# Performance work log

Hardware: AMD Instinct MI355X
Metric: run time of the kernel (lower is better)

The kernel has to match this reference:

```python
import jax, jax.numpy as jnp
import numpy as np

N = 2560          # 64 graphs * 40 nodes (hard-coded by view(64,40,40))
E = 163840        # edges, avg degree 64
HEADS = 4
IN_C = 32
H0 = 128          # hidden_dims[0] per head
H1 = 128          # hidden_dims[1] per head
OUT_E = 40
EPS_BN = 1e-5


def _glorot(key, shape):
    fan = sum(shape[-2:]) if len(shape) > 1 else shape[0]
    return jax.random.normal(key, shape, dtype=jnp.float32) * (2.0 / fan) ** 0.5


def setup_inputs() -> dict:
    key = jax.random.key(0)
    ks = jax.random.split(key, 24)
    inp = {
        "x": jax.random.normal(ks[0], (N, IN_C), dtype=jnp.float32),
        "edge_index": jax.random.randint(ks[1], (2, E), 0, N, dtype=jnp.int32),
        "pos": jax.random.normal(ks[2], (N, 2), dtype=jnp.float32),
        "mask": jax.random.randint(ks[3], (N,), 0, 2, dtype=jnp.int32),
        "adjacency": jax.random.uniform(ks[4], (N, OUT_E), dtype=jnp.float32),
        # GAT layer 1 (in -> heads*H0)
        "W1": _glorot(ks[5], (IN_C, HEADS * H0)),
        "att_src1": _glorot(ks[6], (HEADS, H0)),
        "att_dst1": _glorot(ks[7], (HEADS, H0)),
        "We1": _glorot(ks[8], (1, HEADS * H0)),
        "att_e1": _glorot(ks[9], (HEADS, H0)),
        "bias1": jnp.zeros((HEADS * H0,), dtype=jnp.float32),
        # BatchNorm 1
        "g1": jnp.ones((HEADS * H0,), dtype=jnp.float32),
        "be1": jnp.zeros((HEADS * H0,), dtype=jnp.float32),
        # GAT layer 2 (heads*H0 -> heads*H1)
        "W2": _glorot(ks[10], (HEADS * H0, HEADS * H1)),
        "att_src2": _glorot(ks[11], (HEADS, H1)),
        "att_dst2": _glorot(ks[12], (HEADS, H1)),
        "We2": _glorot(ks[13], (1, HEADS * H1)),
        "att_e2": _glorot(ks[14], (HEADS, H1)),
        "bias2": jnp.zeros((HEADS * H1,), dtype=jnp.float32),
        # BatchNorm 2
        "g2": jnp.ones((HEADS * H1,), dtype=jnp.float32),
        "be2": jnp.zeros((HEADS * H1,), dtype=jnp.float32),
        # fc_edge
        "Wfc": _glorot(ks[15], (HEADS * H1, OUT_E)),
        "bfc": jnp.zeros((OUT_E,), dtype=jnp.float32),
    }
    return inp


def _gat(x, src, dst, ew, W, att_s, att_d, We, att_e, bias, heads, c):
    # x: [N, Fin] -> h: [N, H, C]
    h = (x @ W).reshape(-1, heads, c)
    a_s = (h * att_s).sum(-1)                       # [N, H]
    a_d = (h * att_d).sum(-1)                       # [N, H]
    he = (ew[:, None] @ We).reshape(-1, heads, c)   # [E, H, C] edge attr proj
    a_e = (he * att_e).sum(-1)                      # [E, H]
    alpha = jax.nn.leaky_relu(a_s[src] + a_d[dst] + a_e, 0.2)
    # segment softmax over destination nodes
    m = jax.ops.segment_max(alpha, dst, num_segments=N)
    alpha = jnp.exp(alpha - m[dst])
    denom = jax.ops.segment_sum(alpha, dst, num_segments=N)
    alpha = alpha / (denom[dst] + 1e-16)
    out = jax.ops.segment_sum(h[src] * alpha[:, :, None], dst, num_segments=N)
    return out.reshape(-1, heads * c) + bias


def _batchnorm(x, g, b):
    mu = x.mean(0)
    var = x.var(0)
    return (x - mu) * jax.lax.rsqrt(var + EPS_BN) * g + b


def reference(x, edge_index, pos, mask, adjacency,
              W1, att_src1, att_dst1, We1, att_e1, bias1, g1, be1,
              W2, att_src2, att_dst2, We2, att_e2, bias2, g2, be2,
              Wfc, bfc):
    src, dst = edge_index[0], edge_index[1]
    ew = 1.0 / (jnp.linalg.norm(pos[src] - pos[dst], axis=1) + 1e-6)  # [E]

    h = _gat(x, src, dst, ew, W1, att_src1, att_dst1, We1, att_e1, bias1, HEADS, H0)
    h = jax.nn.relu(_batchnorm(h, g1, be1))

    e = _gat(h, src, dst, ew, W2, att_src2, att_dst2, We2, att_e2, bias2, HEADS, H1)
    e = jax.nn.relu(_batchnorm(e, g2, be2))

    out_edge = e @ Wfc + bfc                     # [N, 40]
    out_edge = out_edge * mask[:, None].astype(out_edge.dtype)
    out_edge = out_edge.reshape(64, 40, 40)
    return out_edge + adjacency.reshape(64, 40, 40)
```

## Files before the change

kernel.cpp:

```cpp
#include <hip/hip_runtime.h>
#include <hip/hip_bf16.h>

#define NN 2560
#define NE 163840
#define NH 4
#define NC 128
#define NF 512
#define OUTE 40
#define CSTR 256

typedef short bf16x8 __attribute__((ext_vector_type(8)));
typedef float f32x4 __attribute__((ext_vector_type(4)));

__device__ inline ushort f2bf(float f) {
    uint u = __float_as_uint(f);
    uint r = u + 0x7FFF + ((u >> 16) & 1);
    return (ushort)(r >> 16);
}
__device__ inline float bflo(uint v) { return __uint_as_float(v << 16); }
__device__ inline float bfhi(uint v) { return __uint_as_float(v & 0xFFFF0000u); }
__device__ inline float bf2f(ushort u) { return __uint_as_float(((uint)u) << 16); }
__device__ inline float rdlanef(float v, int l) {
    return __int_as_float(__builtin_amdgcn_readlane(__float_as_int(v), l));
}
__device__ inline int rdlanei(int v, int l) {
    return __builtin_amdgcn_readlane(v, l);
}
__device__ inline float sel4(float r0, float r1, float r2, float r3, int hd) {
    return (hd & 2) ? ((hd & 1) ? r3 : r2) : ((hd & 1) ? r1 : r0);
}

__global__ __launch_bounds__(256) void k_csr_gemm1(const int* __restrict__ ei,
        const float* __restrict__ pos, int* __restrict__ deg,
        int2* __restrict__ csrp, int* __restrict__ ovf_cnt, int4* __restrict__ ovf,
        const float* __restrict__ We1, const float* __restrict__ ae1,
        const float* __restrict__ We2, const float* __restrict__ ae2,
        float* __restrict__ dote,
        const float* __restrict__ Wfc, ushort* __restrict__ WfcT,
        const float* __restrict__ W2, ushort* __restrict__ W2T,
        const float* __restrict__ x, const float* __restrict__ W1,
        const float* __restrict__ atts, const float* __restrict__ attd,
        ushort* __restrict__ hb, float* __restrict__ as_, float* __restrict__ ad_) {
    __shared__ ushort tile[64][72];
    __shared__ float s_x[4][32];
    __shared__ float4 s_red[4][4];
    int b = blockIdx.x;
    if (b < 640) {
        int e = b * 256 + threadIdx.x;
        int s = ei[e], d = ei[NE + e];
        float dx = pos[2 * s] - pos[2 * d];
        float dy = pos[2 * s + 1] - pos[2 * d + 1];
        float w = 1.0f / (sqrtf(dx * dx + dy * dy) + 1e-6f);
        int r = atomicAdd(&deg[d], 1);
        if (r < CSTR) {
            csrp[(d << 8) + r] = make_int2(s, __float_as_int(w));
        } else {
            int i = atomicAdd(ovf_cnt, 1);
            ovf[i] = make_int4(d, s, __float_as_int(w), 0);
        }
        return;
    }
    if (b < 642) {
        int t = threadIdx.x;
        const float* W = (b == 641) ? We2 : We1;
        const float* A = (b == 641) ? ae2 : ae1;
        int w = t >> 6, l = t & 63;
        float p = W[w * 128 + l] * A[w * 128 + l] + W[w * 128 + 64 + l] * A[w * 128 + 64 + l];
#pragma unroll
        for (int o = 32; o > 0; o >>= 1) p += __shfl_down(p, o);
        if (l == 0) dote[(b - 640) * 4 + w] = p;
        return;
    }
    if (b < 738) {
        int idx = (b - 642) * 256 + threadIdx.x;
        int j = idx >> 9, k = idx & 511;
        WfcT[idx] = (j < OUTE) ? f2bf(Wfc[k * OUTE + j]) : (ushort)0;
        return;
    }
    if (b < 802) {
        int id = b - 738;
        int n0 = (id & 7) * 64, k0 = (id >> 3) * 64;
        int t = threadIdx.x;
        int r = t >> 2, cseg = (t & 3) * 16;
#pragma unroll
        for (int c = 0; c < 16; c += 4) {
            float4 v = *(const float4*)&W2[(k0 + r) * 512 + n0 + cseg + c];
            tile[cseg + c + 0][r] = f2bf(v.x);
            tile[cseg + c + 1][r] = f2bf(v.y);
            tile[cseg + c + 2][r] = f2bf(v.z);
            tile[cseg + c + 3][r] = f2bf(v.w);
        }
        __syncthreads();
        *(uint4*)&W2T[(n0 + r) * 512 + k0 + cseg]     = *(uint4*)&tile[r][cseg];
        *(uint4*)&W2T[(n0 + r) * 512 + k0 + cseg + 8] = *(uint4*)&tile[r][cseg + 8];
        return;
    }
    int n0 = (b - 802) * 4, t = threadIdx.x;
    if (t < 128) s_x[t >> 5][t & 31] = x[n0 * 32 + t];
    __syncthreads();
    float a0[4] = {0.f, 0.f, 0.f, 0.f}, a1[4] = {0.f, 0.f, 0.f, 0.f};
#pragma unroll
    for (int k = 0; k < 32; k++) {
        float w0 = W1[k * 512 + t];
        float w1 = W1[k * 512 + t + 256];
#pragma unroll
        for (int nn = 0; nn < 4; nn++) {
            a0[nn] += s_x[nn][k] * w0;
            a1[nn] += s_x[nn][k] * w1;
        }
    }
    float sa0 = atts[t], sa1 = atts[t + 256];
    float da0 = attd[t], da1 = attd[t + 256];
    int w = t >> 6, lane = t & 63;
#pragma unroll
    for (int nn = 0; nn < 4; nn++) {
        hb[(n0 + nn) * 512 + t] = f2bf(a0[nn]);
        hb[(n0 + nn) * 512 + t + 256] = f2bf(a1[nn]);
        float ps0 = a0[nn] * sa0, pd0 = a0[nn] * da0;
        float ps1 = a1[nn] * sa1, pd1 = a1[nn] * da1;
#pragma unroll
        for (int o = 32; o > 0; o >>= 1) {
            ps0 += __shfl_xor(ps0, o); pd0 += __shfl_xor(pd0, o);
            ps1 += __shfl_xor(ps1, o); pd1 += __shfl_xor(pd1, o);
        }
        if (lane == 0) s_red[w][nn] = make_float4(ps0, pd0, ps1, pd1);
    }
    __syncthreads();
    if (t < 4) {
        int nn = t, n = n0 + nn;
        float4 r0 = s_red[0][nn], r1 = s_red[1][nn], r2 = s_red[2][nn], r3 = s_red[3][nn];
        as_[n * 4 + 0] = r0.x + r1.x; as_[n * 4 + 1] = r2.x + r3.x;
        as_[n * 4 + 2] = r0.z + r1.z; as_[n * 4 + 3] = r2.z + r3.z;
        ad_[n * 4 + 0] = r0.y + r1.y; ad_[n * 4 + 1] = r2.y + r3.y;
        ad_[n * 4 + 2] = r0.w + r1.w; ad_[n * 4 + 3] = r2.w + r3.w;
    }
}

__global__ __launch_bounds__(128) void k_edge_agg(const int* __restrict__ deg_,
        const int2* __restrict__ csrp, const int* __restrict__ ovf_cnt,
        const int4* __restrict__ ovf, const float* __restrict__ as_,
        const float* __restrict__ ad_, const float* __restrict__ dote,
        const ushort* __restrict__ hb, const float* __restrict__ bias,
        ushort* __restrict__ outb) {
    int w = threadIdx.x >> 6, lane = threadIdx.x & 63;
    int n = blockIdx.x * 2 + w;
    int beg = n << 8;
    int degn = deg_[n];
    int dmain = min(degn, CSTR);
    float4 adv = *(const float4*)&ad_[n * 4];
    float4 dv  = *(const float4*)dote;
    float La0 = -1e30f, La1 = -1e30f, La2 = -1e30f, La3 = -1e30f;
    float Lb0 = -1e30f, Lb1 = -1e30f, Lb2 = -1e30f, Lb3 = -1e30f;
    int off0 = 0, off1 = 0;
    if (lane < dmain) {
        int2 p = csrp[beg + lane];
        off0 = p.x * NF;
        float4 a = *(const float4*)&as_[p.x * 4];
        float ww = __int_as_float(p.y);
        float v0 = a.x + adv.x + ww * dv.x; La0 = v0 > 0.f ? v0 : 0.2f * v0;
        float v1 = a.y + adv.y + ww * dv.y; La1 = v1 > 0.f ? v1 : 0.2f * v1;
        float v2 = a.z + adv.z + ww * dv.z; La2 = v2 > 0.f ? v2 : 0.2f * v2;
        float v3 = a.w + adv.w + ww * dv.w; La3 = v3 > 0.f ? v3 : 0.2f * v3;
    }
    if (lane + 64 < dmain) {
        int2 p = csrp[beg + lane + 64];
        off1 = p.x * NF;
        float4 a = *(const float4*)&as_[p.x * 4];
        float ww = __int_as_float(p.y);
        float v0 = a.x + adv.x + ww * dv.x; Lb0 = v0 > 0.f ? v0 : 0.2f * v0;
        float v1 = a.y + adv.y + ww * dv.y; Lb1 = v1 > 0.f ? v1 : 0.2f * v1;
        float v2 = a.z + adv.z + ww * dv.z; Lb2 = v2 > 0.f ? v2 : 0.2f * v2;
        float v3 = a.w + adv.w + ww * dv.w; Lb3 = v3 > 0.f ? v3 : 0.2f * v3;
    }
    float mx0 = fmaxf(La0, Lb0), mx1 = fmaxf(La1, Lb1);
    float mx2 = fmaxf(La2, Lb2), mx3 = fmaxf(La3, Lb3);
    for (int e = 128 + lane; e < dmain; e += 64) {
        int2 p = csrp[beg + e];
        float4 a = *(const float4*)&as_[p.x * 4];
        float ww = __int_as_float(p.y);
        float v0 = a.x + adv.x + ww * dv.x; v0 = v0 > 0.f ? v0 : 0.2f * v0;
        float v1 = a.y + adv.y + ww * dv.y; v1 = v1 > 0.f ? v1 : 0.2f * v1;
        float v2 = a.z + adv.z + ww * dv.z; v2 = v2 > 0.f ? v2 : 0.2f * v2;
        float v3 = a.w + adv.w + ww * dv.w; v3 = v3 > 0.f ? v3 : 0.2f * v3;
        mx0 = fmaxf(mx0, v0); mx1 = fmaxf(mx1, v1);
        mx2 = fmaxf(mx2, v2); mx3 = fmaxf(mx3, v3);
    }
    if (degn > CSTR) {
        int oc = *ovf_cnt;
        for (int i = lane; i < oc; i += 64) {
            int4 o = ovf[i];
            if (o.x == n) {
                float4 a = *(const float4*)&as_[o.y * 4];
                float ww = __int_as_float(o.z);
                float v0 = a.x + adv.x + ww * dv.x; v0 = v0 > 0.f ? v0 : 0.2f * v0;
                float v1 = a.y + adv.y + ww * dv.y; v1 = v1 > 0.f ? v1 : 0.2f * v1;
                float v2 = a.z + adv.z + ww * dv.z; v2 = v2 > 0.f ? v2 : 0.2f * v2;
                float v3 = a.w + adv.w + ww * dv.w; v3 = v3 > 0.f ? v3 : 0.2f * v3;
                mx0 = fmaxf(mx0, v0); mx1 = fmaxf(mx1, v1);
                mx2 = fmaxf(mx2, v2); mx3 = fmaxf(mx3, v3);
            }
        }
    }
#pragma unroll
    for (int o = 32; o > 0; o >>= 1) {
        mx0 = fmaxf(mx0, __shfl_xor(mx0, o));
        mx1 = fmaxf(mx1, __shfl_xor(mx1, o));
        mx2 = fmaxf(mx2, __shfl_xor(mx2, o));
        mx3 = fmaxf(mx3, __shfl_xor(mx3, o));
    }
    float Aa0 = __expf(La0 - mx0), Aa1 = __expf(La1 - mx1);
    float Aa2 = __expf(La2 - mx2), Aa3 = __expf(La3 - mx3);
    float Ab0 = __expf(Lb0 - mx0), Ab1 = __expf(Lb1 - mx1);
    float Ab2 = __expf(Lb2 - mx2), Ab3 = __expf(Lb3 - mx3);
    float s0 = Aa0 + Ab0, s1 = Aa1 + Ab1, s2 = Aa2 + Ab2, s3 = Aa3 + Ab3;
    for (int e = 128 + lane; e < dmain; e += 64) {
        int2 p = csrp[beg + e];
        float4 a = *(const float4*)&as_[p.x * 4];
        float ww = __int_as_float(p.y);
        float v0 = a.x + adv.x + ww * dv.x; v0 = v0 > 0.f ? v0 : 0.2f * v0;
        float v1 = a.y + adv.y + ww * dv.y; v1 = v1 > 0.f ? v1 : 0.2f * v1;
        float v2 = a.z + adv.z + ww * dv.z; v2 = v2 > 0.f ? v2 : 0.2f * v2;
        float v3 = a.w + adv.w + ww * dv.w; v3 = v3 > 0.f ? v3 : 0.2f * v3;
        s0 += __expf(v0 - mx0); s1 += __expf(v1 - mx1);
        s2 += __expf(v2 - mx2); s3 += __expf(v3 - mx3);
    }
    if (degn > CSTR) {
        int oc = *ovf_cnt;
        for (int i = lane; i < oc; i += 64) {
            int4 o = ovf[i];
            if (o.x == n) {
                float4 a = *(const float4*)&as_[o.y * 4];
                float ww = __int_as_float(o.z);
                float v0 = a.x + adv.x + ww * dv.x; v0 = v0 > 0.f ? v0 : 0.2f * v0;
                float v1 = a.y + adv.y + ww * dv.y; v1 = v1 > 0.f ? v1 : 0.2f * v1;
                float v2 = a.z + adv.z + ww * dv.z; v2 = v2 > 0.f ? v2 : 0.2f * v2;
                float v3 = a.w + adv.w + ww * dv.w; v3 = v3 > 0.f ? v3 : 0.2f * v3;
                s0 += __expf(v0 - mx0); s1 += __expf(v1 - mx1);
                s2 += __expf(v2 - mx2); s3 += __expf(v3 - mx3);
            }
        }
    }
#pragma unroll
    for (int o = 32; o > 0; o >>= 1) {
        s0 += __shfl_xor(s0, o); s1 += __shfl_xor(s1, o);
        s2 += __shfl_xor(s2, o); s3 += __shfl_xor(s3, o);
    }
    float inv0 = 1.f / (s0 + 1e-16f), inv1 = 1.f / (s1 + 1e-16f);
    float inv2 = 1.f / (s2 + 1e-16f), inv3 = 1.f / (s3 + 1e-16f);
    int hd = lane >> 4;
    const ushort* hbase = hb + 8 * lane;
    float acc0 = 0.f, acc1 = 0.f, acc2 = 0.f, acc3 = 0.f;
    float acc4 = 0.f, acc5 = 0.f, acc6 = 0.f, acc7 = 0.f;
    int m0 = min(dmain, 64);
    int e = 0;
    for (; e + 8 <= m0; e += 8) {
        int o[8]; float aa[8];
#pragma unroll
        for (int j = 0; j < 8; j++) {
            o[j] = rdlanei(off0, e + j);
            float r0 = rdlanef(Aa0, e + j), r1 = rdlanef(Aa1, e + j);
            float r2 = rdlanef(Aa2, e + j), r3 = rdlanef(Aa3, e + j);
            aa[j] = sel4(r0, r1, r2, r3, hd);
        }
        uint4 v[8];
#pragma unroll
        for (int j = 0; j < 8; j++) v[j] = *(const uint4*)(hbase + o[j]);
#pragma unroll
        for (int j = 0; j < 8; j++) {
            acc0 += aa[j] * bflo(v[j].x); acc1 += aa[j] * bfhi(v[j].x);
            acc2 += aa[j] * bflo(v[j].y); acc3 += aa[j] * bfhi(v[j].y);
            acc4 += aa[j] * bflo(v[j].z); acc5 += aa[j] * bfhi(v[j].z);
            acc6 += aa[j] * bflo(v[j].w); acc7 += aa[j] * bfhi(v[j].w);
        }
    }
    for (; e < m0; e++) {
        float r0 = rdlanef(Aa0, e), r1 = rdlanef(Aa1, e);
        float r2 = rdlanef(Aa2, e), r3 = rdlanef(Aa3, e);
        float a = sel4(r0, r1, r2, r3, hd);
        int o = rdlanei(off0, e);
        uint4 v = *(const uint4*)(hbase + o);
        acc0 += a * bflo(v.x); acc1 += a * bfhi(v.x);
        acc2 += a * bflo(v.y); acc3 += a * bfhi(v.y);
        acc4 += a * bflo(v.z); acc5 += a * bfhi(v.z);
        acc6 += a * bflo(v.w); acc7 += a * bfhi(v.w);
    }
    int m1b = max(min(dmain, 128) - 64, 0);
    e = 0;
    for (; e + 8 <= m1b; e += 8) {
        int o[8]; float aa[8];
#pragma unroll
        for (int j = 0; j < 8; j++) {
            o[j] = rdlanei(off1, e + j);
            float r0 = rdlanef(Ab0, e + j), r1 = rdlanef(Ab1, e + j);
            float r2 = rdlanef(Ab2, e + j), r3 = rdlanef(Ab3, e + j);
            aa[j] = sel4(r0, r1, r2, r3, hd);
        }
        uint4 v[8];
#pragma unroll
        for (int j = 0; j < 8; j++) v[j] = *(const uint4*)(hbase + o[j]);
#pragma unroll
        for (int j = 0; j < 8; j++) {
            acc0 += aa[j] * bflo(v[j].x); acc1 += aa[j] * bfhi(v[j].x);
            acc2 += aa[j] * bflo(v[j].y); acc3 += aa[j] * bfhi(v[j].y);
            acc4 += aa[j] * bflo(v[j].z); acc5 += aa[j] * bfhi(v[j].z);
            acc6 += aa[j] * bflo(v[j].w); acc7 += aa[j] * bfhi(v[j].w);
        }
    }
    for (; e < m1b; e++) {
        float r0 = rdlanef(Ab0, e), r1 = rdlanef(Ab1, e);
        float r2 = rdlanef(Ab2, e), r3 = rdlanef(Ab3, e);
        float a = sel4(r0, r1, r2, r3, hd);
        int o = rdlanei(off1, e);
        uint4 v = *(const uint4*)(hbase + o);
        acc0 += a * bflo(v.x); acc1 += a * bfhi(v.x);
        acc2 += a * bflo(v.y); acc3 += a * bfhi(v.y);
        acc4 += a * bflo(v.z); acc5 += a * bfhi(v.z);
        acc6 += a * bflo(v.w); acc7 += a * bfhi(v.w);
    }
    float adh = sel4(adv.x, adv.y, adv.z, adv.w, hd);
    float dh  = sel4(dv.x, dv.y, dv.z, dv.w, hd);
    float mxh = sel4(mx0, mx1, mx2, mx3, hd);
    for (int ee = 128; ee < dmain; ee++) {
        int2 p = csrp[beg + ee];
        float ash = as_[p.x * 4 + hd];
        float ww = __int_as_float(p.y);
        float vv = ash + adh + ww * dh; vv = vv > 0.f ? vv : 0.2f * vv;
        float a = __expf(vv - mxh);
        uint4 v = *(const uint4*)(hbase + p.x * NF);
        acc0 += a * bflo(v.x); acc1 += a * bfhi(v.x);
        acc2 += a * bflo(v.y); acc3 += a * bfhi(v.y);
        acc4 += a * bflo(v.z); acc5 += a * bfhi(v.z);
        acc6 += a * bflo(v.w); acc7 += a * bfhi(v.w);
    }
    if (degn > CSTR) {
        int oc = *ovf_cnt;
        for (int i = 0; i < oc; i++) {
            int4 o = ovf[i];
            if (o.x == n) {
                float ash = as_[o.y * 4 + hd];
                float ww = __int_as_float(o.z);
                float vv = ash + adh + ww * dh; vv = vv > 0.f ? vv : 0.2f * vv;
                float a = __expf(vv - mxh);
                uint4 v = *(const uint4*)(hbase + o.y * NF);
                acc0 += a * bflo(v.x); acc1 += a * bfhi(v.x);
                acc2 += a * bflo(v.y); acc3 += a * bfhi(v.y);
                acc4 += a * bflo(v.z); acc5 += a * bfhi(v.z);
                acc6 += a * bflo(v.w); acc7 += a * bfhi(v.w);
            }
        }
    }
    float invh = sel4(inv0, inv1, inv2, inv3, hd);
    int ch = 8 * lane;
    float4 b0 = *(const float4*)&bias[ch];
    float4 b1 = *(const float4*)&bias[ch + 4];
    uint4 ov;
    ov.x = (uint)f2bf(acc0 * invh + b0.x) | ((uint)f2bf(acc1 * invh + b0.y) << 16);
    ov.y = (uint)f2bf(acc2 * invh + b0.z) | ((uint)f2bf(acc3 * invh + b0.w) << 16);
    ov.z = (uint)f2bf(acc4 * invh + b1.x) | ((uint)f2bf(acc5 * invh + b1.y) << 16);
    ov.w = (uint)f2bf(acc6 * invh + b1.z) | ((uint)f2bf(acc7 * invh + b1.w) << 16);
    *(uint4*)&outb[n * NF + ch] = ov;
}

__global__ __launch_bounds__(256) void k_bnstats(const ushort* __restrict__ xs,
        float* __restrict__ stats) {
    __shared__ float ps[2048];
    __shared__ float pq[2048];
    int t = threadIdx.x;
    int c8 = (t & 63) * 8, rr = t >> 6;
    float s[8] = {0.f,0.f,0.f,0.f,0.f,0.f,0.f,0.f};
    float q[8] = {0.f,0.f,0.f,0.f,0.f,0.f,0.f,0.f};
#pragma unroll
    for (int rj = 0; rj < 4; rj++) {
        int r = blockIdx.x * 16 + rr * 4 + rj;
        uint4 v = *(const uint4*)&xs[r * NF + c8];
        float vv[8];
        vv[0] = bflo(v.x); vv[1] = bfhi(v.x); vv[2] = bflo(v.y); vv[3] = bfhi(v.y);
        vv[4] = bflo(v.z); vv[5] = bfhi(v.z); vv[6] = bflo(v.w); vv[7] = bfhi(v.w);
#pragma unroll
        for (int c = 0; c < 8; c++) { s[c] += vv[c]; q[c] += vv[c] * vv[c]; }
    }
#pragma unroll
    for (int c = 0; c < 8; c++) {
        ps[rr * 512 + c8 + c] = s[c];
        pq[rr * 512 + c8 + c] = q[c];
    }
    __syncthreads();
    for (int ch = t; ch < 512; ch += 256) {
        atomicAdd(&stats[ch], ps[ch] + ps[512 + ch] + ps[1024 + ch] + ps[1536 + ch]);
        atomicAdd(&stats[NF + ch], pq[ch] + pq[512 + ch] + pq[1024 + ch] + pq[1536 + ch]);
    }
}

__global__ __launch_bounds__(256) void k_gemm2_bn_att(const ushort* __restrict__ Ab,
        const float* __restrict__ stats, const float* __restrict__ g,
        const float* __restrict__ bb, const ushort* __restrict__ BT,
        const float* __restrict__ atts, const float* __restrict__ attd,
        ushort* __restrict__ Cb, float* __restrict__ as_, float* __restrict__ ad_) {
    __shared__ ushort As[64][40];
    __shared__ ushort Bs[128][40];
    __shared__ float s_scale[512], s_shift[512];
    __shared__ float s_ps[2][64], s_pd[2][64];
    int t = threadIdx.x;
    const float invn = 1.0f / (float)NN;
    {
        int j = t;
#pragma unroll
        for (int rep = 0; rep < 2; rep++, j += 256) {
            float mu = stats[j] * invn;
            float var = stats[NF + j] * invn - mu * mu;
            float sc = rsqrtf(var + 1e-5f) * g[j];
            s_scale[j] = sc;
            s_shift[j] = bb[j] - mu * sc;
        }
    }
    int head = blockIdx.x;
    int rowBase = blockIdx.y * 64, colBase = head * 128;
    int w = t >> 6, lane = t & 63;
    int wm = (w >> 1) * 32, wn = (w & 1) * 64;
    int lm = lane & 15, q = lane >> 4;
    f32x4 acc[2][4] = {};
    int sr2 = t >> 2, sk = (t & 3) * 8;
    for (int k0 = 0; k0 < 512; k0 += 32) {
        __syncthreads();
        int jb = k0 + sk;
        float sc[8], sh[8];
#pragma unroll
        for (int c = 0; c < 8; c++) { sc[c] = s_scale[jb + c]; sh[c] = s_shift[jb + c]; }
        uint4 a8 = *(const uint4*)&Ab[(rowBase + sr2) * 512 + jb];
        uint4 b0 = *(const uint4*)&BT[(colBase + sr2) * 512 + jb];
        uint4 b1 = *(const uint4*)&BT[(colBase + 64 + sr2) * 512 + jb];
        ushort pa0[8];
        float av[8];
        av[0] = bflo(a8.x); av[1] = bfhi(a8.x); av[2] = bflo(a8.y); av[3] = bfhi(a8.y);
        av[4] = bflo(a8.z); av[5] = bfhi(a8.z); av[6] = bflo(a8.w); av[7] = bfhi(a8.w);
#pragma unroll
        for (int c = 0; c < 8; c++)
            pa0[c] = f2bf(fmaxf(av[c] * sc[c] + sh[c], 0.f));
        *(uint4*)&As[sr2][sk]      = *(uint4*)pa0;
        *(uint4*)&Bs[sr2][sk]      = b0;
        *(uint4*)&Bs[64 + sr2][sk] = b1;
        __syncthreads();
        bf16x8 af[2], bf[4];
#pragma unroll
        for (int i = 0; i < 2; i++) af[i] = *(const bf16x8*)&As[wm + i * 16 + lm][q * 8];
#pragma unroll
        for (int j = 0; j < 4; j++) bf[j] = *(const bf16x8*)&Bs[wn + j * 16 + lm][q * 8];
#pragma unroll
        for (int i = 0; i < 2; i++)
#pragma unroll
            for (int j = 0; j < 4; j++)
                acc[i][j] = __builtin_amdgcn_mfma_f32_16x16x32_bf16(af[i], bf[j], acc[i][j], 0, 0, 0);
    }
#pragma unroll
    for (int i = 0; i < 2; i++) {
        int row = rowBase + wm + i * 16 + q * 4;
#pragma unroll
        for (int j = 0; j < 4; j++) {
            int col = colBase + wn + j * 16 + lm;
#pragma unroll
            for (int r = 0; r < 4; r++)
                Cb[(row + r) * 512 + col] = f2bf(acc[i][j][r]);
        }
    }
    float sa[4], da[4];
#pragma unroll
    for (int j = 0; j < 4; j++) {
        int col = colBase + wn + j * 16 + lm;
        sa[j] = atts[col]; da[j] = attd[col];
    }
#pragma unroll
    for (int i = 0; i < 2; i++) {
#pragma unroll
        for (int r = 0; r < 4; r++) {
            float ps = 0.f, pd = 0.f;
#pragma unroll
            for (int j = 0; j < 4; j++) {
                float c = acc[i][j][r];
                ps += c * sa[j]; pd += c * da[j];
            }
#pragma unroll
            for (int o = 1; o < 16; o <<= 1) { ps += __shfl_xor(ps, o); pd += __shfl_xor(pd, o); }
            if (lm == 0) {
                int row = wm + i * 16 + q * 4 + r;
                s_ps[w & 1][row] = ps; s_pd[w & 1][row] = pd;
            }
        }
    }
    __syncthreads();
    if (t < 64) {
        as_[(rowBase + t) * 4 + head] = s_ps[0][t] + s_ps[1][t];
    } else if (t < 128) {
        int row = t - 64;
        ad_[(rowBase + row) * 4 + head] = s_pd[0][row] + s_pd[1][row];
    }
}

__global__ __launch_bounds__(256) void k_fc_bn(const ushort* __restrict__ e2b,
        const float* __restrict__ stats, const float* __restrict__ g,
        const float* __restrict__ bb, const ushort* __restrict__ WfcT,
        const float* __restrict__ bfc, const int* __restrict__ mask,
        const float* __restrict__ adj, float* __restrict__ out) {
    __shared__ float s_scale[512], s_shift[512];
    __shared__ f32x4 s_acc[3][64][3];
    int t = threadIdx.x;
    int w = t >> 6, lane = t & 63;
    const float invn = 1.0f / (float)NN;
#pragma unroll
    for (int j = t; j < 512; j += 256) {
        float mu = stats[j] * invn;
        float var = stats[NF + j] * invn - mu * mu;
        float sc = rsqrtf(var + 1e-5f) * g[j];
        s_scale[j] = sc;
        s_shift[j] = bb[j] - mu * sc;
    }
    __syncthreads();
    int r0 = blockIdx.x * 16;
    int lm = lane & 15, q = lane >> 4;
    f32x4 acc[3] = {};
#pragma unroll
    for (int kk = 0; kk < 4; kk++) {
        int k0 = w * 128 + kk * 32;
        int jb = k0 + q * 8;
        uint4 a8 = *(const uint4*)&e2b[(r0 + lm) * 512 + jb];
        float av[8];
        av[0] = bflo(a8.x); av[1] = bfhi(a8.x); av[2] = bflo(a8.y); av[3] = bfhi(a8.y);
        av[4] = bflo(a8.z); av[5] = bfhi(a8.z); av[6] = bflo(a8.w); av[7] = bfhi(a8.w);
        ushort pa[8];
#pragma unroll
        for (int c = 0; c < 8; c++)
            pa[c] = f2bf(fmaxf(av[c] * s_scale[jb + c] + s_shift[jb + c], 0.f));
        bf16x8 af = *(const bf16x8*)pa;
#pragma unroll
        for (int jt = 0; jt < 3; jt++) {
            bf16x8 bf = *(const bf16x8*)&WfcT[(jt * 16 + lm) * 512 + k0 + q * 8];
            acc[jt] = __builtin_amdgcn_mfma_f32_16x16x32_bf16(af, bf, acc[jt], 0, 0, 0);
        }
    }
    if (w > 0) {
#pragma unroll
        for (int jt = 0; jt < 3; jt++) s_acc[w - 1][lane][jt] = acc[jt];
    }
    __syncthreads();
    if (w == 0) {
#pragma unroll
        for (int jt = 0; jt < 3; jt++) {
            acc[jt] += s_acc[0][lane][jt] + s_acc[1][lane][jt] + s_acc[2][lane][jt];
            int col = jt * 16 + lm;
            if (col < OUTE) {
#pragma unroll
                for (int r = 0; r < 4; r++) {
                    int n = r0 + q * 4 + r;
                    float v = acc[jt][r] + bfc[col];
                    v = mask[n] ? v : 0.f;
                    out[n * OUTE + col] = v + adj[n * OUTE + col];
                }
            }
        }
    }
}

extern "C" void kernel_launch(void* const* d_in, const int* in_sizes, int n_in,
                              void* d_out, int out_size, void* d_ws, size_t ws_size,
                              hipStream_t stream) {
    const float* x       = (const float*)d_in[0];
    const int*   ei      = (const int*)d_in[1];
    const float* pos     = (const float*)d_in[2];
    const int*   mask    = (const int*)d_in[3];
    const float* adj     = (const float*)d_in[4];
    const float* W1      = (const float*)d_in[5];
    const float* atts1   = (const float*)d_in[6];
    const float* attd1   = (const float*)d_in[7];
    const float* We1     = (const float*)d_in[8];
    const float* atte1   = (const float*)d_in[9];
    const float* bias1   = (const float*)d_in[10];
    const float* g1      = (const float*)d_in[11];
    const float* be1     = (const float*)d_in[12];
    const float* W2      = (const float*)d_in[13];
    const float* atts2   = (const float*)d_in[14];
    const float* attd2   = (const float*)d_in[15];
    const float* We2     = (const float*)d_in[16];
    const float* atte2   = (const float*)d_in[17];
    const float* bias2   = (const float*)d_in[18];
    const float* g2      = (const float*)d_in[19];
    const float* be2     = (const float*)d_in[20];
    const float* Wfc     = (const float*)d_in[21];
    const float* bfc     = (const float*)d_in[22];
    float* out = (float*)d_out;

    char* ws = (char*)d_ws;
    int*    deg     = (int*)(ws);
    int*    ovf_cnt = (int*)(ws + 2560 * 4);
    float*  stats   = (float*)(ws + 5120 * 4);
    float*  dote    = (float*)(ws + 7168 * 4);
    int2*   csrp    = (int2*)(ws + 7184 * 4);
    int4*   ovf     = (int4*)(ws + 1317904 * 4);
    float*  as_     = (float*)(ws + 1973264 * 4);
    float*  ad_     = (float*)(ws + 1983504 * 4);
    ushort* t1b     = (ushort*)(ws + 1993744 * 4);
    ushort* hb      = (ushort*)(ws + 2649104 * 4);
    ushort* W2T     = (ushort*)(ws + 3304464 * 4);
    ushort* WfcT    = (ushort*)(ws + 3435536 * 4);

    hipMemsetAsync(d_ws, 0, 7168 * 4, stream);

    k_csr_gemm1<<<802 + NN / 4, 256, 0, stream>>>(ei, pos, deg, csrp, ovf_cnt, ovf,
                                                  We1, atte1, We2, atte2, dote,
                                                  Wfc, WfcT, W2, W2T,
                                                  x, W1, atts1, attd1, hb, as_, ad_);

    k_edge_agg<<<NN / 2, 128, 0, stream>>>(deg, csrp, ovf_cnt, ovf, as_, ad_,
                                           dote, hb, bias1, t1b);
    k_bnstats<<<NN / 16, 256, 0, stream>>>(t1b, stats);

    k_gemm2_bn_att<<<dim3(4, NN / 64), 256, 0, stream>>>(t1b, stats, g1, be1, W2T,
                                                         atts2, attd2, hb, as_, ad_);
    k_edge_agg<<<NN / 2, 128, 0, stream>>>(deg, csrp, ovf_cnt, ovf, as_, ad_,
                                           dote + 4, hb, bias2, t1b);
    k_bnstats<<<NN / 16, 256, 0, stream>>>(t1b, stats + 1024);

    k_fc_bn<<<NN / 16, 256, 0, stream>>>(t1b, stats + 1024, g2, be2, WfcT, bfc, mask, adj, out);
}
```

Baseline: 196.0 us.

## Fuse BN stats into consumer kernels via atomic counter spin-wait; stage alpha in LDS

The BatchNorm statistics kernels are merged into the following GEMM2 and FC kernels. The first 160 blocks compute the stats and bump an agent-scope done counter. The remaining blocks spin-wait on that counter, then read the stats with atomic loads, which removes two kernel launches. In edge aggregation, the CSR loads are hoisted and made unconditional with clamped indices, attention weights are staged in shared memory instead of being fetched with readlane and select per edge, and the first gather loop is unrolled to 16. The spin-wait relies on the stats blocks being scheduled before or alongside the waiting blocks, which risks deadlock or stalls if they are not.

Measured after the change: 209.3 us. 1.07x slower.

```diff
diff --git a/kernel.cpp b/kernel.cpp
--- a/kernel.cpp
+++ b/kernel.cpp
@@ -142,36 +142,41 @@
         const float* __restrict__ ad_, const float* __restrict__ dote,
         const ushort* __restrict__ hb, const float* __restrict__ bias,
         ushort* __restrict__ outb) {
+    __shared__ float s_alpha[2][2][4][72];
     int w = threadIdx.x >> 6, lane = threadIdx.x & 63;
     int n = blockIdx.x * 2 + w;
     int beg = n << 8;
+    int2 p0 = csrp[beg + lane];
+    int2 p1 = csrp[beg + 64 + lane];
     int degn = deg_[n];
-    int dmain = min(degn, CSTR);
     float4 adv = *(const float4*)&ad_[n * 4];
     float4 dv  = *(const float4*)dote;
-    float La0 = -1e30f, La1 = -1e30f, La2 = -1e30f, La3 = -1e30f;
-    float Lb0 = -1e30f, Lb1 = -1e30f, Lb2 = -1e30f, Lb3 = -1e30f;
-    int off0 = 0, off1 = 0;
-    if (lane < dmain) {
-        int2 p = csrp[beg + lane];
-        off0 = p.x * NF;
-        float4 a = *(const float4*)&as_[p.x * 4];
-        float ww = __int_as_float(p.y);
-        float v0 = a.x + adv.x + ww * dv.x; La0 = v0 > 0.f ? v0 : 0.2f * v0;
-        float v1 = a.y + adv.y + ww * dv.y; La1 = v1 > 0.f ? v1 : 0.2f * v1;
-        float v2 = a.z + adv.z + ww * dv.z; La2 = v2 > 0.f ? v2 : 0.2f * v2;
-        float v3 = a.w + adv.w + ww * dv.w; La3 = v3 > 0.f ? v3 : 0.2f * v3;
-    }
-    if (lane + 64 < dmain) {
-        int2 p = csrp[beg + lane + 64];
-        off1 = p.x * NF;
-        float4 a = *(const float4*)&as_[p.x * 4];
-        float ww = __int_as_float(p.y);
-        float v0 = a.x + adv.x + ww * dv.x; Lb0 = v0 > 0.f ? v0 : 0.2f * v0;
-        float v1 = a.y + adv.y + ww * dv.y; Lb1 = v1 > 0.f ? v1 : 0.2f * v1;
-        float v2 = a.z + adv.z + ww * dv.z; Lb2 = v2 > 0.f ? v2 : 0.2f * v2;
-        float v3 = a.w + adv.w + ww * dv.w; Lb3 = v3 > 0.f ? v3 : 0.2f * v3;
-    }
+    int i0 = min(max(p0.x, 0), NN - 1);
+    int i1 = min(max(p1.x, 0), NN - 1);
+    float4 a0 = *(const float4*)&as_[i0 * 4];
+    float4 a1 = *(const float4*)&as_[i1 * 4];
+    int dmain = min(degn, CSTR);
+    bool val0 = lane < dmain, val1 = lane + 64 < dmain;
+    float ww0 = __int_as_float(p0.y), ww1 = __int_as_float(p1.y);
+    float La0, La1, La2, La3, Lb0, Lb1, Lb2, Lb3;
+    {
+        float v0 = a0.x + adv.x + ww0 * dv.x; v0 = v0 > 0.f ? v0 : 0.2f * v0;
+        float v1 = a0.y + adv.y + ww0 * dv.y; v1 = v1 > 0.f ? v1 : 0.2f * v1;
+        float v2 = a0.z + adv.z + ww0 * dv.z; v2 = v2 > 0.f ? v2 : 0.2f * v2;
+        float v3 = a0.w + adv.w + ww0 * dv.w; v3 = v3 > 0.f ? v3 : 0.2f * v3;
+        La0 = val0 ? v0 : -1e30f; La1 = val0 ? v1 : -1e30f;
+        La2 = val0 ? v2 : -1e30f; La3 = val0 ? v3 : -1e30f;
+    }
+    {
+        float v0 = a1.x + adv.x + ww1 * dv.x; v0 = v0 > 0.f ? v0 : 0.2f * v0;
+        float v1 = a1.y + adv.y + ww1 * dv.y; v1 = v1 > 0.f ? v1 : 0.2f * v1;
+        float v2 = a1.z + adv.z + ww1 * dv.z; v2 = v2 > 0.f ? v2 : 0.2f * v2;
+        float v3 = a1.w + adv.w + ww1 * dv.w; v3 = v3 > 0.f ? v3 : 0.2f * v3;
+        Lb0 = val1 ? v0 : -1e30f; Lb1 = val1 ? v1 : -1e30f;
+        Lb2 = val1 ? v2 : -1e30f; Lb3 = val1 ? v3 : -1e30f;
+    }
+    int off0 = val0 ? i0 * NF : 0;
+    int off1 = val1 ? i1 * NF : 0;
     float mx0 = fmaxf(La0, Lb0), mx1 = fmaxf(La1, Lb1);
     float mx2 = fmaxf(La2, Lb2), mx3 = fmaxf(La3, Lb3);
     for (int e = 128 + lane; e < dmain; e += 64) {
@@ -247,36 +252,34 @@
     }
     float inv0 = 1.f / (s0 + 1e-16f), inv1 = 1.f / (s1 + 1e-16f);
     float inv2 = 1.f / (s2 + 1e-16f), inv3 = 1.f / (s3 + 1e-16f);
+    s_alpha[w][0][0][lane] = Aa0; s_alpha[w][0][1][lane] = Aa1;
+    s_alpha[w][0][2][lane] = Aa2; s_alpha[w][0][3][lane] = Aa3;
+    s_alpha[w][1][0][lane] = Ab0; s_alpha[w][1][1][lane] = Ab1;
+    s_alpha[w][1][2][lane] = Ab2; s_alpha[w][1][3][lane] = Ab3;
     int hd = lane >> 4;
     const ushort* hbase = hb + 8 * lane;
     float acc0 = 0.f, acc1 = 0.f, acc2 = 0.f, acc3 = 0.f;
     float acc4 = 0.f, acc5 = 0.f, acc6 = 0.f, acc7 = 0.f;
     int m0 = min(dmain, 64);
     int e = 0;
-    for (; e + 8 <= m0; e += 8) {
-        int o[8]; float aa[8];
-#pragma unroll
-        for (int j = 0; j < 8; j++) {
-            o[j] = rdlanei(off0, e + j);
-            float r0 = rdlanef(Aa0, e + j), r1 = rdlanef(Aa1, e + j);
-            float r2 = rdlanef(Aa2, e + j), r3 = rdlanef(Aa3, e + j);
-            aa[j] = sel4(r0, r1, r2, r3, hd);
-        }
-        uint4 v[8];
-#pragma unroll
-        for (int j = 0; j < 8; j++) v[j] = *(const uint4*)(hbase + o[j]);
-#pragma unroll
-        for (int j = 0; j < 8; j++) {
-            acc0 += aa[j] * bflo(v[j].x); acc1 += aa[j] * bfhi(v[j].x);
-            acc2 += aa[j] * bflo(v[j].y); acc3 += aa[j] * bfhi(v[j].y);
-            acc4 += aa[j] * bflo(v[j].z); acc5 += aa[j] * bfhi(v[j].z);
-            acc6 += aa[j] * bflo(v[j].w); acc7 += aa[j] * bfhi(v[j].w);
+    for (; e + 16 <= m0; e += 16) {
+        int o[16];
+#pragma unroll
+        for (int j = 0; j < 16; j++) o[j] = rdlanei(off0, e + j);
+        uint4 v[16];
+#pragma unroll
+        for (int j = 0; j < 16; j++) v[j] = *(const uint4*)(hbase + o[j]);
+#pragma unroll
+        for (int j = 0; j < 16; j++) {
+            float a = s_alpha[w][0][hd][e + j];
+            acc0 += a * bflo(v[j].x); acc1 += a * bfhi(v[j].x);
+            acc2 += a * bflo(v[j].y); acc3 += a * bfhi(v[j].y);
+            acc4 += a * bflo(v[j].z); acc5 += a * bfhi(v[j].z);
+            acc6 += a * bflo(v[j].w); acc7 += a * bfhi(v[j].w);
         }
     }
     for (; e < m0; e++) {
-        float r0 = rdlanef(Aa0, e), r1 = rdlanef(Aa1, e);
-        float r2 = rdlanef(Aa2, e), r3 = rdlanef(Aa3, e);
-        float a = sel4(r0, r1, r2, r3, hd);
+        float a = s_alpha[w][0][hd][e];
         int o = rdlanei(off0, e);
         uint4 v = *(const uint4*)(hbase + o);
         acc0 += a * bflo(v.x); acc1 += a * bfhi(v.x);
@@ -287,29 +290,23 @@
     int m1b = max(min(dmain, 128) - 64, 0);
     e = 0;
     for (; e + 8 <= m1b; e += 8) {
-        int o[8]; float aa[8];
+        int o[8];
+#pragma unroll
+        for (int j = 0; j < 8; j++) o[j] = rdlanei(off1, e + j);
+        uint4 v[8];
+#pragma unroll
+        for (int j = 0; j < 8; j++) v[j] = *(const uint4*)(hbase + o[j]);
 #pragma unroll
         for (int j = 0; j < 8; j++) {
-            o[j] = rdlanei(off1, e + j);
-            float r0 = rdlanef(Ab0, e + j), r1 = rdlanef(Ab1, e + j);
-            float r2 = rdlanef(Ab2, e + j), r3 = rdlanef(Ab3, e + j);
-            aa[j] = sel4(r0, r1, r2, r3, hd);
-        }
-        uint4 v[8];
-#pragma unroll
-        for (int j = 0; j < 8; j++) v[j] = *(const uint4*)(hbase + o[j]);
-#pragma unroll
-        for (int j = 0; j < 8; j++) {
-            acc0 += aa[j] * bflo(v[j].x); acc1 += aa[j] * bfhi(v[j].x);
-            acc2 += aa[j] * bflo(v[j].y); acc3 += aa[j] * bfhi(v[j].y);
-            acc4 += aa[j] * bflo(v[j].z); acc5 += aa[j] * bfhi(v[j].z);
-            acc6 += aa[j] * bflo(v[j].w); acc7 += aa[j] * bfhi(v[j].w);
+            float a = s_alpha[w][1][hd][e + j];
+            acc0 += a * bflo(v[j].x); acc1 += a * bfhi(v[j].x);
+            acc2 += a * bflo(v[j].y); acc3 += a * bfhi(v[j].y);
+            acc4 += a * bflo(v[j].z); acc5 += a * bfhi(v[j].z);
+            acc6 += a * bflo(v[j].w); acc7 += a * bfhi(v[j].w);
         }
     }
     for (; e < m1b; e++) {
-        float r0 = rdlanef(Ab0, e), r1 = rdlanef(Ab1, e);
-        float r2 = rdlanef(Ab2, e), r3 = rdlanef(Ab3, e);
-        float a = sel4(r0, r1, r2, r3, hd);
+        float a = s_alpha[w][1][hd][e];
         int o = rdlanei(off1, e);
         uint4 v = *(const uint4*)(hbase + o);
         acc0 += a * bflo(v.x); acc1 += a * bfhi(v.x);
@@ -361,10 +358,10 @@
     *(uint4*)&outb[n * NF + ch] = ov;
 }
 
-__global__ __launch_bounds__(256) void k_bnstats(const ushort* __restrict__ xs,
-        float* __restrict__ stats) {
-    __shared__ float ps[2048];
-    __shared__ float pq[2048];
+__device__ __forceinline__ void bnstats_body(char* smem, const ushort* __restrict__ xs,
+        float* __restrict__ stats, int* done) {
+    float* ps = (float*)smem;
+    float* pq = (float*)(smem + 8192);
     int t = threadIdx.x;
     int c8 = (t & 63) * 8, rr = t >> 6;
     float s[8] = {0.f,0.f,0.f,0.f,0.f,0.f,0.f,0.f};
@@ -389,32 +386,52 @@
         atomicAdd(&stats[ch], ps[ch] + ps[512 + ch] + ps[1024 + ch] + ps[1536 + ch]);
         atomicAdd(&stats[NF + ch], pq[ch] + pq[512 + ch] + pq[1024 + ch] + pq[1536 + ch]);
     }
-}
-
-__global__ __launch_bounds__(256) void k_gemm2_bn_att(const ushort* __restrict__ Ab,
-        const float* __restrict__ stats, const float* __restrict__ g,
+    __syncthreads();
+    if (t == 0)
+        __hip_atomic_fetch_add(done, 1, __ATOMIC_RELEASE, __HIP_MEMORY_SCOPE_AGENT);
+}
+
+__device__ __forceinline__ void wait_done(const int* done, int target) {
+    if (threadIdx.x == 0) {
+        while (__hip_atomic_load((int*)done, __ATOMIC_ACQUIRE, __HIP_MEMORY_SCOPE_AGENT) < target)
+            __builtin_amdgcn_s_sleep(8);
+    }
+    __syncthreads();
+}
+__device__ __forceinline__ float ld_agent(const float* p) {
+    return __hip_atomic_load((float*)p, __ATOMIC_RELAXED, __HIP_MEMORY_SCOPE_AGENT);
+}
+
+__global__ __launch_bounds__(256) void k_stats_gemm2(const ushort* __restrict__ Ab,
+        float* __restrict__ stats, int* done, const float* __restrict__ g,
         const float* __restrict__ bb, const ushort* __restrict__ BT,
         const float* __restrict__ atts, const float* __restrict__ attd,
         ushort* __restrict__ Cb, float* __restrict__ as_, float* __restrict__ ad_) {
-    __shared__ ushort As[64][40];
-    __shared__ ushort Bs[128][40];
-    __shared__ float s_scale[512], s_shift[512];
-    __shared__ float s_ps[2][64], s_pd[2][64];
+    __shared__ __align__(16) char smem[20480];
+    if (blockIdx.x < 160) { bnstats_body(smem, Ab, stats, done); return; }
+    int b2 = blockIdx.x - 160;
+    ushort (*As)[40] = (ushort(*)[40])smem;
+    ushort (*Bs)[40] = (ushort(*)[40])(smem + 5120);
+    float* s_scale   = (float*)(smem + 15360);
+    float* s_shift   = (float*)(smem + 17408);
+    float (*s_ps)[64] = (float(*)[64])(smem + 19456);
+    float (*s_pd)[64] = (float(*)[64])(smem + 19968);
     int t = threadIdx.x;
     const float invn = 1.0f / (float)NN;
+    wait_done(done, 160);
     {
         int j = t;
 #pragma unroll
         for (int rep = 0; rep < 2; rep++, j += 256) {
-            float mu = stats[j] * invn;
-            float var = stats[NF + j] * invn - mu * mu;
+            float mu = ld_agent(&stats[j]) * invn;
+            float var = ld_agent(&stats[NF + j]) * invn - mu * mu;
             float sc = rsqrtf(var + 1e-5f) * g[j];
             s_scale[j] = sc;
             s_shift[j] = bb[j] - mu * sc;
         }
     }
-    int head = blockIdx.x;
-    int rowBase = blockIdx.y * 64, colBase = head * 128;
+    int head = b2 & 3;
+    int rowBase = (b2 >> 2) * 64, colBase = head * 128;
     int w = t >> 6, lane = t & 63;
     int wm = (w >> 1) * 32, wn = (w & 1) * 64;
     int lm = lane & 15, q = lane >> 4;
@@ -495,26 +512,31 @@
     }
 }
 
-__global__ __launch_bounds__(256) void k_fc_bn(const ushort* __restrict__ e2b,
-        const float* __restrict__ stats, const float* __restrict__ g,
+__global__ __launch_bounds__(256) void k_stats_fc(const ushort* __restrict__ e2b,
+        float* __restrict__ stats, int* done, const float* __restrict__ g,
         const float* __restrict__ bb, const ushort* __restrict__ WfcT,
         const float* __restrict__ bfc, const int* __restrict__ mask,
         const float* __restrict__ adj, float* __restrict__ out) {
-    __shared__ float s_scale[512], s_shift[512];
-    __shared__ f32x4 s_acc[3][64][3];
+    __shared__ __align__(16) char smem[16384];
+    if (blockIdx.x < 160) { bnstats_body(smem, e2b, stats, done); return; }
+    int b2 = blockIdx.x - 160;
+    float* s_scale = (float*)smem;
+    float* s_shift = (float*)(smem + 2048);
+    f32x4 (*s_acc)[64][3] = (f32x4(*)[64][3])(smem + 4096);
     int t = threadIdx.x;
     int w = t >> 6, lane = t & 63;
     const float invn = 1.0f / (float)NN;
+    wait_done(done, 160);
 #pragma unroll
     for (int j = t; j < 512; j += 256) {
-        float mu = stats[j] * invn;
-        float var = stats[NF + j] * invn - mu * mu;
+        float mu = ld_agent(&stats[j]) * invn;
+        float var = ld_agent(&stats[NF + j]) * invn - mu * mu;
         float sc = rsqrtf(var + 1e-5f) * g[j];
         s_scale[j] = sc;
         s_shift[j] = bb[j] - mu * sc;
     }
     __syncthreads();
-    int r0 = blockIdx.x * 16;
+    int r0 = b2 * 16;
     int lm = lane & 15, q = lane >> 4;
     f32x4 acc[3] = {};
 #pragma unroll
@@ -590,6 +612,8 @@
     char* ws = (char*)d_ws;
     int*    deg     = (int*)(ws);
     int*    ovf_cnt = (int*)(ws + 2560 * 4);
+    int*    done1   = (int*)(ws + 2576 * 4);
+    int*    done2   = (int*)(ws + 2592 * 4);
     float*  stats   = (float*)(ws + 5120 * 4);
     float*  dote    = (float*)(ws + 7168 * 4);
     int2*   csrp    = (int2*)(ws + 7184 * 4);
@@ -610,13 +634,10 @@
 
     k_edge_agg<<<NN / 2, 128, 0, stream>>>(deg, csrp, ovf_cnt, ovf, as_, ad_,
                                            dote, hb, bias1, t1b);
-    k_bnstats<<<NN / 16, 256, 0, stream>>>(t1b, stats);
-
-    k_gemm2_bn_att<<<dim3(4, NN / 64), 256, 0, stream>>>(t1b, stats, g1, be1, W2T,
-                                                         atts2, attd2, hb, as_, ad_);
+    k_stats_gemm2<<<320, 256, 0, stream>>>(t1b, stats, done1, g1, be1, W2T,
+                                           atts2, attd2, hb, as_, ad_);
     k_edge_agg<<<NN / 2, 128, 0, stream>>>(deg, csrp, ovf_cnt, ovf, as_, ad_,
                                            dote + 4, hb, bias2, t1b);
-    k_bnstats<<<NN / 16, 256, 0, stream>>>(t1b, stats + 1024);
-
-    k_fc_bn<<<NN / 16, 256, 0, stream>>>(t1b, stats + 1024, g2, be2, WfcT, bfc, mask, adj, out);
-}
+    k_stats_fc<<<320, 256, 0, stream>>>(t1b, stats + 1024, done2, g2, be2,
+                                        WfcT, bfc, mask, adj, out);
+}
```

## Fuse BN-stats kernels into consumer kernels with atomic completion counter

Applied to the files above, without the earlier changes.

The standalone batch-norm statistics kernels are merged into the following GEMM2 and FC kernels. The first 160 blocks compute the statistics and bump a done counter with release semantics, and the remaining blocks spin-wait on that counter before reading the stats with agent-scope loads. This removes two kernel launches and their launch gaps. It relies on the stats blocks being scheduled before or alongside the waiting blocks; that holds for a 320-block grid on this GPU, but an inter-block spin wait is fragile in general.

After: 214.9 us. +9.6%, slower.

```diff
diff --git a/kernel.cpp b/kernel.cpp
--- a/kernel.cpp
+++ b/kernel.cpp
@@ -361,10 +361,10 @@
     *(uint4*)&outb[n * NF + ch] = ov;
 }
 
-__global__ __launch_bounds__(256) void k_bnstats(const ushort* __restrict__ xs,
-        float* __restrict__ stats) {
-    __shared__ float ps[2048];
-    __shared__ float pq[2048];
+__device__ __forceinline__ void bnstats_body(char* smem, const ushort* __restrict__ xs,
+        float* __restrict__ stats, int* done) {
+    float* ps = (float*)smem;
+    float* pq = (float*)(smem + 8192);
     int t = threadIdx.x;
     int c8 = (t & 63) * 8, rr = t >> 6;
     float s[8] = {0.f,0.f,0.f,0.f,0.f,0.f,0.f,0.f};
@@ -389,32 +389,52 @@
         atomicAdd(&stats[ch], ps[ch] + ps[512 + ch] + ps[1024 + ch] + ps[1536 + ch]);
         atomicAdd(&stats[NF + ch], pq[ch] + pq[512 + ch] + pq[1024 + ch] + pq[1536 + ch]);
     }
-}
-
-__global__ __launch_bounds__(256) void k_gemm2_bn_att(const ushort* __restrict__ Ab,
-        const float* __restrict__ stats, const float* __restrict__ g,
+    __syncthreads();
+    if (t == 0)
+        __hip_atomic_fetch_add(done, 1, __ATOMIC_RELEASE, __HIP_MEMORY_SCOPE_AGENT);
+}
+
+__device__ __forceinline__ void wait_done(const int* done, int target) {
+    if (threadIdx.x == 0) {
+        while (__hip_atomic_load((int*)done, __ATOMIC_ACQUIRE, __HIP_MEMORY_SCOPE_AGENT) < target)
+            __builtin_amdgcn_s_sleep(8);
+    }
+    __syncthreads();
+}
+__device__ __forceinline__ float ld_agent(const float* p) {
+    return __hip_atomic_load((float*)p, __ATOMIC_RELAXED, __HIP_MEMORY_SCOPE_AGENT);
+}
+
+__global__ __launch_bounds__(256) void k_stats_gemm2(const ushort* __restrict__ Ab,
+        float* __restrict__ stats, int* done, const float* __restrict__ g,
         const float* __restrict__ bb, const ushort* __restrict__ BT,
         const float* __restrict__ atts, const float* __restrict__ attd,
         ushort* __restrict__ Cb, float* __restrict__ as_, float* __restrict__ ad_) {
-    __shared__ ushort As[64][40];
-    __shared__ ushort Bs[128][40];
-    __shared__ float s_scale[512], s_shift[512];
-    __shared__ float s_ps[2][64], s_pd[2][64];
+    __shared__ __align__(16) char smem[20480];
+    if (blockIdx.x < 160) { bnstats_body(smem, Ab, stats, done); return; }
+    int b2 = blockIdx.x - 160;
+    ushort (*As)[40] = (ushort(*)[40])smem;
+    ushort (*Bs)[40] = (ushort(*)[40])(smem + 5120);
+    float* s_scale   = (float*)(smem + 15360);
+    float* s_shift   = (float*)(smem + 17408);
+    float (*s_ps)[64] = (float(*)[64])(smem + 19456);
+    float (*s_pd)[64] = (float(*)[64])(smem + 19968);
     int t = threadIdx.x;
     const float invn = 1.0f / (float)NN;
+    wait_done(done, 160);
     {
         int j = t;
 #pragma unroll
         for (int rep = 0; rep < 2; rep++, j += 256) {
-            float mu = stats[j] * invn;
-            float var = stats[NF + j] * invn - mu * mu;
+            float mu = ld_agent(&stats[j]) * invn;
+            float var = ld_agent(&stats[NF + j]) * invn - mu * mu;
             float sc = rsqrtf(var + 1e-5f) * g[j];
             s_scale[j] = sc;
             s_shift[j] = bb[j] - mu * sc;
         }
     }
-    int head = blockIdx.x;
-    int rowBase = blockIdx.y * 64, colBase = head * 128;
+    int head = b2 & 3;
+    int rowBase = (b2 >> 2) * 64, colBase = head * 128;
     int w = t >> 6, lane = t & 63;
     int wm = (w >> 1) * 32, wn = (w & 1) * 64;
     int lm = lane & 15, q = lane >> 4;
@@ -495,26 +515,31 @@
     }
 }
 
-__global__ __launch_bounds__(256) void k_fc_bn(const ushort* __restrict__ e2b,
-        const float* __restrict__ stats, const float* __restrict__ g,
+__global__ __launch_bounds__(256) void k_stats_fc(const ushort* __restrict__ e2b,
+        float* __restrict__ stats, int* done, const float* __restrict__ g,
         const float* __restrict__ bb, const ushort* __restrict__ WfcT,
         const float* __restrict__ bfc, const int* __restrict__ mask,
         const float* __restrict__ adj, float* __restrict__ out) {
-    __shared__ float s_scale[512], s_shift[512];
-    __shared__ f32x4 s_acc[3][64][3];
+    __shared__ __align__(16) char smem[16384];
+    if (blockIdx.x < 160) { bnstats_body(smem, e2b, stats, done); return; }
+    int b2 = blockIdx.x - 160;
+    float* s_scale = (float*)smem;
+    float* s_shift = (float*)(smem + 2048);
+    f32x4 (*s_acc)[64][3] = (f32x4(*)[64][3])(smem + 4096);
     int t = threadIdx.x;
     int w = t >> 6, lane = t & 63;
     const float invn = 1.0f / (float)NN;
+    wait_done(done, 160);
 #pragma unroll
     for (int j = t; j < 512; j += 256) {
-        float mu = stats[j] * invn;
-        float var = stats[NF + j] * invn - mu * mu;
+        float mu = ld_agent(&stats[j]) * invn;
+        float var = ld_agent(&stats[NF + j]) * invn - mu * mu;
         float sc = rsqrtf(var + 1e-5f) * g[j];
         s_scale[j] = sc;
         s_shift[j] = bb[j] - mu * sc;
     }
     __syncthreads();
-    int r0 = blockIdx.x * 16;
+    int r0 = b2 * 16;
     int lm = lane & 15, q = lane >> 4;
     f32x4 acc[3] = {};
 #pragma unroll
@@ -590,6 +615,8 @@
     char* ws = (char*)d_ws;
     int*    deg     = (int*)(ws);
     int*    ovf_cnt = (int*)(ws + 2560 * 4);
+    int*    done1   = (int*)(ws + 2576 * 4);
+    int*    done2   = (int*)(ws + 2592 * 4);
     float*  stats   = (float*)(ws + 5120 * 4);
     float*  dote    = (float*)(ws + 7168 * 4);
     int2*   csrp    = (int2*)(ws + 7184 * 4);
@@ -610,13 +637,10 @@
 
     k_edge_agg<<<NN / 2, 128, 0, stream>>>(deg, csrp, ovf_cnt, ovf, as_, ad_,
                                            dote, hb, bias1, t1b);
-    k_bnstats<<<NN / 16, 256, 0, stream>>>(t1b, stats);
-
-    k_gemm2_bn_att<<<dim3(4, NN / 64), 256, 0, stream>>>(t1b, stats, g1, be1, W2T,
-                                                         atts2, attd2, hb, as_, ad_);
+    k_stats_gemm2<<<320, 256, 0, stream>>>(t1b, stats, done1, g1, be1, W2T,
+                                           atts2, attd2, hb, as_, ad_);
     k_edge_agg<<<NN / 2, 128, 0, stream>>>(deg, csrp, ovf_cnt, ovf, as_, ad_,
                                            dote + 4, hb, bias2, t1b);
-    k_bnstats<<<NN / 16, 256, 0, stream>>>(t1b, stats + 1024);
-
-    k_fc_bn<<<NN / 16, 256, 0, stream>>>(t1b, stats + 1024, g2, be2, WfcT, bfc, mask, adj, out);
-}
+    k_stats_fc<<<320, 256, 0, stream>>>(t1b, stats + 1024, done2, g2, be2,
+                                        WfcT, bfc, mask, adj, out);
+}
```
